# Kernel optimization log

Measured on AMD Instinct MI355X. Metric: run time of the kernel, lower is better.

## Reference

```python
import jax, jax.numpy as jnp
import numpy as np

N_NODES = 100000
D_IN = 128
D_OUT = 128
SHAPES = {"r1": 1, "r2": 2, "r3": 3}
N_EDGES = {"r1": 400000, "r2": 300000, "r3": 200000}


def setup_inputs() -> dict:
    key = jax.random.key(0)
    ks = jax.random.split(key, 10)
    inp = {
        "x": jax.random.normal(ks[0], (N_NODES, D_IN), dtype=jnp.float32),
        "A_r1": jax.random.normal(ks[1], (D_IN * 1, D_OUT), dtype=jnp.float32) * 0.05,
        "A_r2": jax.random.normal(ks[2], (D_IN * 2, D_OUT), dtype=jnp.float32) * 0.05,
        "A_r3": jax.random.normal(ks[3], (D_IN * 3, D_OUT), dtype=jnp.float32) * 0.05,
        "C_w": jax.random.normal(ks[4], (D_IN, D_OUT), dtype=jnp.float32) * 0.05,
        "C_b": jax.random.normal(ks[5], (D_OUT,), dtype=jnp.float32) * 0.05,
    }
    for j, (name, shape) in enumerate(SHAPES.items()):
        n = N_EDGES[name] * shape
        inp[f"ei_{name}"] = jax.random.randint(ks[6 + j], (2, n), 0, N_NODES, dtype=jnp.int64)
    return inp


def _edge_type_agg(x, edge_indices, A, shape):
    # edge_indices: [2, n_edges*shape]; row0 = sources, row1 reshaped -> dest per hyperedge
    dest = edge_indices[1].reshape(-1, shape)[:, 0]          # [n_edges]
    gathered = x[edge_indices[0]].reshape(-1, shape * x.shape[1])  # [n_edges, shape*D_IN]
    msg = gathered @ A                                        # [n_edges, D_OUT]
    # 1/count(dest) normalization (torch.unique counts == per-type in-degree)
    deg = jax.ops.segment_sum(jnp.ones_like(dest, dtype=msg.dtype), dest, num_segments=x.shape[0])
    msg = msg / deg[dest][:, None]
    return jax.ops.segment_sum(msg, dest, num_segments=x.shape[0])  # scatter_add


def reference(x, ei_r1, ei_r2, ei_r3, A_r1, A_r2, A_r3, C_w, C_b):
    agg = (_edge_type_agg(x, ei_r1, A_r1, 1)
           + _edge_type_agg(x, ei_r2, A_r2, 2)
           + _edge_type_agg(x, ei_r3, A_r3, 3))
    return x @ C_w + C_b + agg
```

## Files before the change

kernel.cpp:

```cpp
#include <hip/hip_runtime.h>

#define N_NODES 100000
#define D 128
#define NND 12800000
#define NTOT (3 * N_NODES)

typedef unsigned short u16;
typedef short s16x8 __attribute__((ext_vector_type(8)));
typedef float f32x4 __attribute__((ext_vector_type(4)));


__device__ __forceinline__ u16 f2b(float f) {
    union { float f; unsigned u; } v; v.f = f;
    unsigned r = (v.u + 0x7FFFu + ((v.u >> 16) & 1u)) >> 16;
    return (u16)r;
}


__global__ __launch_bounds__(256) void convert_all(
    const float* __restrict__ A1, const float* __restrict__ A2,
    const float* __restrict__ A3, const float* __restrict__ Cw,
    u16* __restrict__ ATb) {
    int m = blockIdx.x >> 6;
    int idx = (blockIdx.x & 63) * 256 + threadIdx.x;
    int n = idx >> 7, kk = idx & 127;
    const float* src; int srow;
    if (m == 0)      { src = Cw; srow = kk; }
    else if (m == 1) { src = A1; srow = kk; }
    else if (m < 4)  { src = A2; srow = (m - 2) * 128 + kk; }
    else             { src = A3; srow = (m - 4) * 128 + kk; }
    ATb[m * 16384 + n * 128 + kk] = f2b(src[(long)srow * 128 + n]);
}


__global__ __launch_bounds__(256) void zero_deg(int* deg, int n) {
    int i = blockIdx.x * 256 + threadIdx.x;
    if (i < n) deg[i] = 0;
}

__global__ __launch_bounds__(256) void deg_count(const int* __restrict__ ei, int n_edges,
                                                 int shape, int* __restrict__ deg) {
    int e = blockIdx.x * 256 + threadIdx.x;
    if (e < n_edges) {
        int dest = ei[(long)n_edges * shape + (long)e * shape];
        atomicAdd(&deg[dest], 1);
    }
}

__global__ __launch_bounds__(256) void scan_reduce(const int* __restrict__ deg,
                                                   int* __restrict__ bsums, int n) {
    __shared__ int s[256];
    int t = threadIdx.x;
    int base = blockIdx.x * 1024 + t * 4;
    int loc = 0;
#pragma unroll
    for (int r = 0; r < 4; r++) {
        int idx = base + r;
        if (idx < n) loc += deg[idx];
    }
    s[t] = loc;
    for (int off = 128; off > 0; off >>= 1) {
        __syncthreads();
        if (t < off) s[t] += s[t + off];
    }
    if (t == 0) bsums[blockIdx.x] = s[0];
}

__global__ __launch_bounds__(512) void scan_tops(const int* __restrict__ bsums,
                                                 int* __restrict__ boffs,
                                                 int* __restrict__ offs, int nb, int n) {
    __shared__ int s[512];
    int t = threadIdx.x;
    int v = (t < nb) ? bsums[t] : 0;
    s[t] = v;
    for (int off = 1; off < 512; off <<= 1) {
        __syncthreads();
        int x = (t >= off) ? s[t - off] : 0;
        __syncthreads();
        s[t] += x;
    }
    if (t < nb) boffs[t] = s[t] - v;
    if (t == nb - 1) offs[n] = s[t];
}

__global__ __launch_bounds__(256) void scan_final(const int* __restrict__ deg,
                                                  const int* __restrict__ boffs,
                                                  int* __restrict__ offs,
                                                  int* __restrict__ cursor, int n) {
    __shared__ int s[256];
    int t = threadIdx.x;
    int base = blockIdx.x * 1024 + t * 4;
    int v[4], p[4];
#pragma unroll
    for (int r = 0; r < 4; r++) {
        int idx = base + r;
        v[r] = (idx < n) ? deg[idx] : 0;
    }
    p[0] = 0; p[1] = v[0]; p[2] = v[0] + v[1]; p[3] = v[0] + v[1] + v[2];
    int tsum = p[3] + v[3];
    s[t] = tsum;
    for (int off = 1; off < 256; off <<= 1) {
        __syncthreads();
        int x = (t >= off) ? s[t - off] : 0;
        __syncthreads();
        s[t] += x;
    }
    int texcl = s[t] - tsum + boffs[blockIdx.x];
#pragma unroll
    for (int r = 0; r < 4; r++) {
        int idx = base + r;
        if (idx < n) {
            int val = texcl + p[r];
            offs[idx] = val;
            cursor[idx] = val;
        }
    }
}

template <int SHAPE>
__global__ __launch_bounds__(256) void scatter_src(const int* __restrict__ ei, int n_edges,
                                                   int* __restrict__ cursor, int base,
                                                   int* __restrict__ csr) {
    int e = blockIdx.x * 256 + threadIdx.x;
    if (e < n_edges) {
        int dest = ei[(long)n_edges * SHAPE + (long)e * SHAPE];
        int pos = atomicAdd(&cursor[dest], 1) - base;
#pragma unroll
        for (int s = 0; s < SHAPE; s++) csr[pos * SHAPE + s] = ei[(long)e * SHAPE + s];
    }
}


template <int NW, bool DENSE>
__global__ __launch_bounds__(256) void gemm_y(
    const float* __restrict__ x, const u16* __restrict__ AT,
    const float* __restrict__ Cb, u16* __restrict__ Yout, float* __restrict__ outf) {
    __shared__ u16 Xs[4][64][40];
    const int t = threadIdx.x;
    const int d0 = blockIdx.x * 64;

#pragma unroll
    for (int i = 0; i < 8; i++) {
        int f = i * 256 + t;
        int row = f >> 5;
        int k4 = f & 31;
        int rs = d0 + row < N_NODES ? d0 + row : N_NODES - 1;
        float4 v = *(const float4*)&x[(long)rs * D + k4 * 4];
        int chunk = k4 >> 3, kk = (k4 & 7) * 4;
        u16* p = &Xs[chunk][row][kk];
        p[0] = f2b(v.x); p[1] = f2b(v.y); p[2] = f2b(v.z); p[3] = f2b(v.w);
    }
    __syncthreads();

    const int lane = t & 63, wv = t >> 6;
    const int nbase = wv * 32, quad = lane >> 4, lrow = lane & 15;

    s16x8 afrag[4][4];
#pragma unroll
    for (int mi = 0; mi < 4; mi++)
#pragma unroll
        for (int c = 0; c < 4; c++)
            afrag[mi][c] = *(const s16x8*)&Xs[c][mi * 16 + lrow][quad * 8];

#pragma unroll
    for (int w = 0; w < NW; w++) {
        const u16* B = AT + w * 16384;
        s16x8 bfrag[2][4];
#pragma unroll
        for (int ni = 0; ni < 2; ni++)
#pragma unroll
            for (int c = 0; c < 4; c++)
                bfrag[ni][c] = *(const s16x8*)(B + (long)(nbase + ni * 16 + lrow) * 128 +
                                               c * 32 + quad * 8);
        f32x4 acc[4][2];
#pragma unroll
        for (int mi = 0; mi < 4; mi++)
#pragma unroll
            for (int ni = 0; ni < 2; ni++) acc[mi][ni] = (f32x4)(0.0f);
#pragma unroll
        for (int c = 0; c < 4; c++)
#pragma unroll
            for (int mi = 0; mi < 4; mi++)
#pragma unroll
                for (int ni = 0; ni < 2; ni++)
                    acc[mi][ni] = __builtin_amdgcn_mfma_f32_16x16x32_bf16(
                        afrag[mi][c], bfrag[ni][c], acc[mi][ni], 0, 0, 0);
#pragma unroll
        for (int mi = 0; mi < 4; mi++)
#pragma unroll
            for (int ni = 0; ni < 2; ni++)
#pragma unroll
                for (int reg = 0; reg < 4; reg++) {
                    int row = mi * 16 + quad * 4 + reg;
                    int col = nbase + ni * 16 + lrow;
                    if (d0 + row < N_NODES) {
                        long idx = (long)(d0 + row) * D + col;
                        if (DENSE) outf[idx] = acc[mi][ni][reg] + Cb[col];
                        else Yout[(long)w * NND + idx] = f2b(acc[mi][ni][reg]);
                    }
                }
    }
}


template <int SHAPE>
__global__ __launch_bounds__(256) void gather_acc(
    const u16* __restrict__ Y, const int* __restrict__ csr,
    const int* __restrict__ offs_t, int base, float* __restrict__ out) {
    const int lane = threadIdx.x & 63;
    int wid = blockIdx.x * 4 + (threadIdx.x >> 6);
    const int nw = gridDim.x * 4;
    for (int d = wid; d < N_NODES; d += nw) {
        int lo = offs_t[d] - base;
        int hi = offs_t[d + 1] - base;
        int cnt = hi - lo;
        if (cnt <= 0) continue;
        float a0 = 0.0f, a1 = 0.0f;
        int p = lo;
        for (; p + 4 <= hi; p += 4) {
            int sv[4][SHAPE];
#pragma unroll
            for (int i = 0; i < 4; i++)
#pragma unroll
                for (int s = 0; s < SHAPE; s++) sv[i][s] = csr[(p + i) * SHAPE + s];
            unsigned rw[4][SHAPE];
#pragma unroll
            for (int i = 0; i < 4; i++)
#pragma unroll
                for (int s = 0; s < SHAPE; s++)
                    rw[i][s] = *(const unsigned*)(Y + (long)s * NND +
                                                  (long)sv[i][s] * D + lane * 2);
#pragma unroll
            for (int i = 0; i < 4; i++)
#pragma unroll
                for (int s = 0; s < SHAPE; s++) {
                    a0 += __uint_as_float(rw[i][s] << 16);
                    a1 += __uint_as_float(rw[i][s] & 0xFFFF0000u);
                }
        }
        for (; p < hi; p++) {
            int sv[SHAPE];
#pragma unroll
            for (int s = 0; s < SHAPE; s++) sv[s] = csr[p * SHAPE + s];
#pragma unroll
            for (int s = 0; s < SHAPE; s++) {
                unsigned w = *(const unsigned*)(Y + (long)s * NND + (long)sv[s] * D + lane * 2);
                a0 += __uint_as_float(w << 16);
                a1 += __uint_as_float(w & 0xFFFF0000u);
            }
        }
        float inv = 1.0f / (float)cnt;
        float2* op = (float2*)&out[(long)d * D + lane * 2];
        float2 o = *op;
        o.x += a0 * inv;
        o.y += a1 * inv;
        *op = o;
    }
}


extern "C" void kernel_launch(void* const* d_in, const int* in_sizes, int n_in,
                              void* d_out, int out_size, void* d_ws, size_t ws_size,
                              hipStream_t stream) {
    const float* x  = (const float*)d_in[0];
    const float* A1 = (const float*)d_in[1];
    const float* A2 = (const float*)d_in[2];
    const float* A3 = (const float*)d_in[3];
    const float* Cw = (const float*)d_in[4];
    const float* Cb = (const float*)d_in[5];
    const int* e1 = (const int*)d_in[6];
    const int* e2 = (const int*)d_in[7];
    const int* e3 = (const int*)d_in[8];
    float* out = (float*)d_out;

    int* ws = (int*)d_ws;
    int* deg    = ws;
    int* offs   = ws + 300000;
    int* cursor = ws + 600001;
    int* csr1   = ws + 900001;
    int* csr2   = ws + 1300001;
    int* csr3   = ws + 1900001;
    int* bsums  = ws + 2500001;
    int* boffs  = ws + 2500513;

    u16* ATb = (u16*)((char*)d_ws + 10004224);
    u16* ATCw = ATb;
    u16* AT1  = ATb + 16384;
    u16* AT2  = ATb + 32768;
    u16* AT3  = ATb + 65536;
    u16* Y    = (u16*)((char*)d_ws + 10233600);

    const int NE1 = in_sizes[6] / 2;
    const int NE2 = in_sizes[7] / (2 * 2);
    const int NE3 = in_sizes[8] / (2 * 3);
    const int n = NTOT;
    const int NB = (n + 1023) / 1024;
    const int GB = (N_NODES + 63) / 64;

    convert_all<<<448, 256, 0, stream>>>(A1, A2, A3, Cw, ATb);

    zero_deg<<<(n + 255) / 256, 256, 0, stream>>>(deg, n);
    deg_count<<<(NE1 + 255) / 256, 256, 0, stream>>>(e1, NE1, 1, deg);
    deg_count<<<(NE2 + 255) / 256, 256, 0, stream>>>(e2, NE2, 2, deg + N_NODES);
    deg_count<<<(NE3 + 255) / 256, 256, 0, stream>>>(e3, NE3, 3, deg + 2 * N_NODES);

    scan_reduce<<<NB, 256, 0, stream>>>(deg, bsums, n);
    scan_tops<<<1, 512, 0, stream>>>(bsums, boffs, offs, NB, n);
    scan_final<<<NB, 256, 0, stream>>>(deg, boffs, offs, cursor, n);

    scatter_src<1><<<(NE1 + 255) / 256, 256, 0, stream>>>(e1, NE1, cursor, 0, csr1);
    scatter_src<2><<<(NE2 + 255) / 256, 256, 0, stream>>>(e2, NE2, cursor + N_NODES, NE1, csr2);
    scatter_src<3><<<(NE3 + 255) / 256, 256, 0, stream>>>(e3, NE3, cursor + 2 * N_NODES,
                                                          NE1 + NE2, csr3);

    gemm_y<1, true><<<GB, 256, 0, stream>>>(x, ATCw, Cb, nullptr, out);

    gemm_y<1, false><<<GB, 256, 0, stream>>>(x, AT1, nullptr, Y, nullptr);
    gather_acc<1><<<2048, 256, 0, stream>>>(Y, csr1, offs, 0, out);

    gemm_y<2, false><<<GB, 256, 0, stream>>>(x, AT2, nullptr, Y, nullptr);
    gather_acc<2><<<2048, 256, 0, stream>>>(Y, csr2, offs + N_NODES, NE1, out);

    gemm_y<3, false><<<GB, 256, 0, stream>>>(x, AT3, nullptr, Y, nullptr);
    gather_acc<3><<<2048, 256, 0, stream>>>(Y, csr3, offs + 2 * N_NODES, NE1 + NE2, out);
}
```

Baseline: 438.0 us.

## Unify per-type CSR into one weighted entry list and fuse GEMMs and gathers

Replaces the three per-type CSR builds, four GEMMs and three gather passes with one combined CSR per destination node. Each entry carries a precomputed 1/deg scale, and the x@C_w term is added as a self-entry with weight 1. A single GEMM kernel computes all seven weight slices and writes bf16 Y with coalesced stores staged through shared memory. A single gather then produces each output row in one write with the bias added. This removes repeated read-modify-write of the output, several kernel launches, and the fp32 dense GEMM output path. In exchange the dense C_w term is now rounded through bf16, entries are 8 bytes, and Y grows to seven slabs.

Result: faster. 356.6 us (-18.6%).

```diff
diff --git a/kernel.cpp b/kernel.cpp
--- a/kernel.cpp
+++ b/kernel.cpp
@@ -2,53 +2,73 @@
 
 #define N_NODES 100000
 #define D 128
-#define NND 12800000
-#define NTOT (3 * N_NODES)
+#define NND 12800000L
 
 typedef unsigned short u16;
 typedef short s16x8 __attribute__((ext_vector_type(8)));
 typedef float f32x4 __attribute__((ext_vector_type(4)));
 
+
+#define ENTS_OFF 2004160L
+#define AT_OFF   15604224L
+#define Y_OFF    15833600L
 
 __device__ __forceinline__ u16 f2b(float f) {
     union { float f; unsigned u; } v; v.f = f;
     unsigned r = (v.u + 0x7FFFu + ((v.u >> 16) & 1u)) >> 16;
     return (u16)r;
 }
-
-
-__global__ __launch_bounds__(256) void convert_all(
+__device__ __forceinline__ float blo(unsigned w) { return __uint_as_float(w << 16); }
+__device__ __forceinline__ float bhi(unsigned w) { return __uint_as_float(w & 0xFFFF0000u); }
+
+
+__global__ __launch_bounds__(256) void init_kernel(
     const float* __restrict__ A1, const float* __restrict__ A2,
     const float* __restrict__ A3, const float* __restrict__ Cw,
-    u16* __restrict__ ATb) {
-    int m = blockIdx.x >> 6;
-    int idx = (blockIdx.x & 63) * 256 + threadIdx.x;
+    u16* __restrict__ ATb, int* __restrict__ deg) {
+    int b = blockIdx.x, t = threadIdx.x;
+    if (b < 293) {
+        int i0 = (b * 256 + t) * 4;
+#pragma unroll
+        for (int r = 0; r < 4; r++)
+            if (i0 + r < 300000) deg[i0 + r] = 0;
+        return;
+    }
+    int mb = b - 293;
+    int m = mb >> 6;
+    int idx = (mb & 63) * 256 + t;
     int n = idx >> 7, kk = idx & 127;
     const float* src; int srow;
-    if (m == 0)      { src = Cw; srow = kk; }
-    else if (m == 1) { src = A1; srow = kk; }
-    else if (m < 4)  { src = A2; srow = (m - 2) * 128 + kk; }
-    else             { src = A3; srow = (m - 4) * 128 + kk; }
+    if (m == 0)      { src = A1; srow = kk; }
+    else if (m < 3)  { src = A2; srow = (m - 1) * 128 + kk; }
+    else if (m < 6)  { src = A3; srow = (m - 3) * 128 + kk; }
+    else             { src = Cw; srow = kk; }
     ATb[m * 16384 + n * 128 + kk] = f2b(src[(long)srow * 128 + n]);
 }
 
 
-__global__ __launch_bounds__(256) void zero_deg(int* deg, int n) {
-    int i = blockIdx.x * 256 + threadIdx.x;
-    if (i < n) deg[i] = 0;
-}
-
-__global__ __launch_bounds__(256) void deg_count(const int* __restrict__ ei, int n_edges,
-                                                 int shape, int* __restrict__ deg) {
-    int e = blockIdx.x * 256 + threadIdx.x;
-    if (e < n_edges) {
-        int dest = ei[(long)n_edges * shape + (long)e * shape];
-        atomicAdd(&deg[dest], 1);
-    }
-}
-
-__global__ __launch_bounds__(256) void scan_reduce(const int* __restrict__ deg,
-                                                   int* __restrict__ bsums, int n) {
+__global__ __launch_bounds__(256) void deg_all(
+    const int* __restrict__ e1, const int* __restrict__ e2, const int* __restrict__ e3,
+    int ne1, int ne2, int ne3, int* __restrict__ deg) {
+    int g = blockIdx.x * 256 + threadIdx.x;
+    if (g < ne1) {
+        atomicAdd(&deg[e1[ne1 + g]], 1);
+    } else if (g < ne1 + ne2) {
+        int e = g - ne1;
+        atomicAdd(&deg[N_NODES + e2[ne2 * 2 + e * 2]], 1);
+    } else if (g < ne1 + ne2 + ne3) {
+        int e = g - ne1 - ne2;
+        atomicAdd(&deg[2 * N_NODES + e3[ne3 * 3 + e * 3]], 1);
+    }
+}
+
+__device__ __forceinline__ int ucnt(const int* deg, int d) {
+    return 1 + deg[d] + 2 * deg[N_NODES + d] + 3 * deg[2 * N_NODES + d];
+}
+
+
+__global__ __launch_bounds__(256) void scan_reduce_u(const int* __restrict__ deg,
+                                                     int* __restrict__ bsums, int n) {
     __shared__ int s[256];
     int t = threadIdx.x;
     int base = blockIdx.x * 1024 + t * 4;
@@ -56,7 +76,7 @@
 #pragma unroll
     for (int r = 0; r < 4; r++) {
         int idx = base + r;
-        if (idx < n) loc += deg[idx];
+        if (idx < n) loc += ucnt(deg, idx);
     }
     s[t] = loc;
     for (int off = 128; off > 0; off >>= 1) {
@@ -83,10 +103,9 @@
     if (t == nb - 1) offs[n] = s[t];
 }
 
-__global__ __launch_bounds__(256) void scan_final(const int* __restrict__ deg,
-                                                  const int* __restrict__ boffs,
-                                                  int* __restrict__ offs,
-                                                  int* __restrict__ cursor, int n) {
+__global__ __launch_bounds__(256) void scan_final_u(
+    const int* __restrict__ deg, const int* __restrict__ boffs,
+    int* __restrict__ offs, int* __restrict__ cursor, int2* __restrict__ ents, int n) {
     __shared__ int s[256];
     int t = threadIdx.x;
     int base = blockIdx.x * 1024 + t * 4;
@@ -94,7 +113,7 @@
 #pragma unroll
     for (int r = 0; r < 4; r++) {
         int idx = base + r;
-        v[r] = (idx < n) ? deg[idx] : 0;
+        v[r] = (idx < n) ? ucnt(deg, idx) : 0;
     }
     p[0] = 0; p[1] = v[0]; p[2] = v[0] + v[1]; p[3] = v[0] + v[1] + v[2];
     int tsum = p[3] + v[3];
@@ -112,30 +131,48 @@
         if (idx < n) {
             int val = texcl + p[r];
             offs[idx] = val;
-            cursor[idx] = val;
+            cursor[idx] = val + 1;
+            ents[val] = make_int2(6 * N_NODES + idx, __float_as_int(1.0f));
         }
     }
 }
 
-template <int SHAPE>
-__global__ __launch_bounds__(256) void scatter_src(const int* __restrict__ ei, int n_edges,
-                                                   int* __restrict__ cursor, int base,
-                                                   int* __restrict__ csr) {
-    int e = blockIdx.x * 256 + threadIdx.x;
-    if (e < n_edges) {
-        int dest = ei[(long)n_edges * SHAPE + (long)e * SHAPE];
-        int pos = atomicAdd(&cursor[dest], 1) - base;
-#pragma unroll
-        for (int s = 0; s < SHAPE; s++) csr[pos * SHAPE + s] = ei[(long)e * SHAPE + s];
-    }
-}
-
-
-template <int NW, bool DENSE>
-__global__ __launch_bounds__(256) void gemm_y(
-    const float* __restrict__ x, const u16* __restrict__ AT,
-    const float* __restrict__ Cb, u16* __restrict__ Yout, float* __restrict__ outf) {
-    __shared__ u16 Xs[4][64][40];
+
+__global__ __launch_bounds__(256) void scatter_all(
+    const int* __restrict__ e1, const int* __restrict__ e2, const int* __restrict__ e3,
+    int ne1, int ne2, int ne3, const int* __restrict__ deg,
+    int* __restrict__ cursor, int2* __restrict__ ents) {
+    int g = blockIdx.x * 256 + threadIdx.x;
+    if (g < ne1) {
+        int dest = e1[ne1 + g];
+        float sc = 1.0f / (float)deg[dest];
+        int pos = atomicAdd(&cursor[dest], 1);
+        ents[pos] = make_int2(e1[g], __float_as_int(sc));
+    } else if (g < ne1 + ne2) {
+        int e = g - ne1;
+        int dest = e2[ne2 * 2 + e * 2];
+        float sc = 1.0f / (float)deg[N_NODES + dest];
+        int pos = atomicAdd(&cursor[dest], 2);
+        ents[pos]     = make_int2(1 * N_NODES + e2[e * 2],     __float_as_int(sc));
+        ents[pos + 1] = make_int2(2 * N_NODES + e2[e * 2 + 1], __float_as_int(sc));
+    } else if (g < ne1 + ne2 + ne3) {
+        int e = g - ne1 - ne2;
+        int dest = e3[ne3 * 3 + e * 3];
+        float sc = 1.0f / (float)deg[2 * N_NODES + dest];
+        int pos = atomicAdd(&cursor[dest], 3);
+#pragma unroll
+        for (int s = 0; s < 3; s++)
+            ents[pos + s] = make_int2((3 + s) * N_NODES + e3[e * 3 + s], __float_as_int(sc));
+    }
+}
+
+
+__global__ __launch_bounds__(256) void gemm_all(
+    const float* __restrict__ x, const u16* __restrict__ AT, u16* __restrict__ Y) {
+    __shared__ float smemf[64 * 132];
+    typedef u16 XsT[64][40];
+    XsT* Xs = reinterpret_cast<XsT*>(smemf);
+
     const int t = threadIdx.x;
     const int d0 = blockIdx.x * 64;
 
@@ -162,8 +199,7 @@
         for (int c = 0; c < 4; c++)
             afrag[mi][c] = *(const s16x8*)&Xs[c][mi * 16 + lrow][quad * 8];
 
-#pragma unroll
-    for (int w = 0; w < NW; w++) {
+    for (int w = 0; w < 7; w++) {
         const u16* B = AT + w * 16384;
         s16x8 bfrag[2][4];
 #pragma unroll
@@ -185,6 +221,8 @@
                 for (int ni = 0; ni < 2; ni++)
                     acc[mi][ni] = __builtin_amdgcn_mfma_f32_16x16x32_bf16(
                         afrag[mi][c], bfrag[ni][c], acc[mi][ni], 0, 0, 0);
+
+        __syncthreads();
 #pragma unroll
         for (int mi = 0; mi < 4; mi++)
 #pragma unroll
@@ -193,68 +231,62 @@
                 for (int reg = 0; reg < 4; reg++) {
                     int row = mi * 16 + quad * 4 + reg;
                     int col = nbase + ni * 16 + lrow;
-                    if (d0 + row < N_NODES) {
-                        long idx = (long)(d0 + row) * D + col;
-                        if (DENSE) outf[idx] = acc[mi][ni][reg] + Cb[col];
-                        else Yout[(long)w * NND + idx] = f2b(acc[mi][ni][reg]);
-                    }
+                    smemf[row * 132 + col] = acc[mi][ni][reg];
                 }
-    }
-}
-
-
-template <int SHAPE>
-__global__ __launch_bounds__(256) void gather_acc(
-    const u16* __restrict__ Y, const int* __restrict__ csr,
-    const int* __restrict__ offs_t, int base, float* __restrict__ out) {
-    const int lane = threadIdx.x & 63;
-    int wid = blockIdx.x * 4 + (threadIdx.x >> 6);
-    const int nw = gridDim.x * 4;
-    for (int d = wid; d < N_NODES; d += nw) {
-        int lo = offs_t[d] - base;
-        int hi = offs_t[d + 1] - base;
-        int cnt = hi - lo;
-        if (cnt <= 0) continue;
-        float a0 = 0.0f, a1 = 0.0f;
-        int p = lo;
-        for (; p + 4 <= hi; p += 4) {
-            int sv[4][SHAPE];
-#pragma unroll
-            for (int i = 0; i < 4; i++)
-#pragma unroll
-                for (int s = 0; s < SHAPE; s++) sv[i][s] = csr[(p + i) * SHAPE + s];
-            unsigned rw[4][SHAPE];
-#pragma unroll
-            for (int i = 0; i < 4; i++)
-#pragma unroll
-                for (int s = 0; s < SHAPE; s++)
-                    rw[i][s] = *(const unsigned*)(Y + (long)s * NND +
-                                                  (long)sv[i][s] * D + lane * 2);
-#pragma unroll
-            for (int i = 0; i < 4; i++)
-#pragma unroll
-                for (int s = 0; s < SHAPE; s++) {
-                    a0 += __uint_as_float(rw[i][s] << 16);
-                    a1 += __uint_as_float(rw[i][s] & 0xFFFF0000u);
-                }
-        }
-        for (; p < hi; p++) {
-            int sv[SHAPE];
-#pragma unroll
-            for (int s = 0; s < SHAPE; s++) sv[s] = csr[p * SHAPE + s];
-#pragma unroll
-            for (int s = 0; s < SHAPE; s++) {
-                unsigned w = *(const unsigned*)(Y + (long)s * NND + (long)sv[s] * D + lane * 2);
-                a0 += __uint_as_float(w << 16);
-                a1 += __uint_as_float(w & 0xFFFF0000u);
+        __syncthreads();
+        u16* Yw = Y + (long)w * NND;
+#pragma unroll
+        for (int i = 0; i < 8; i++) {
+            int f = i * 256 + t;
+            int row = f >> 5;
+            int col = (f & 31) * 4;
+            if (d0 + row < N_NODES) {
+                float4 v = *(const float4*)&smemf[row * 132 + col];
+                unsigned o0 = (unsigned)f2b(v.x) | ((unsigned)f2b(v.y) << 16);
+                unsigned o1 = (unsigned)f2b(v.z) | ((unsigned)f2b(v.w) << 16);
+                uint2 o = make_uint2(o0, o1);
+                *(uint2*)(Yw + (long)(d0 + row) * D + col) = o;
             }
         }
-        float inv = 1.0f / (float)cnt;
-        float2* op = (float2*)&out[(long)d * D + lane * 2];
-        float2 o = *op;
-        o.x += a0 * inv;
-        o.y += a1 * inv;
-        *op = o;
+        __syncthreads();
+    }
+}
+
+
+__global__ __launch_bounds__(256) void gather_all(
+    const u16* __restrict__ Y, const int2* __restrict__ ents,
+    const int* __restrict__ offs, const float* __restrict__ Cb,
+    float* __restrict__ out) {
+    const int lane = threadIdx.x & 63;
+    const int wv = __builtin_amdgcn_readfirstlane(threadIdx.x >> 6);
+    int wid = blockIdx.x * 4 + wv;
+    const int nw = gridDim.x * 4;
+    const float cb0 = Cb[lane * 2];
+    const float cb1 = Cb[lane * 2 + 1];
+
+    for (int d = wid; d < N_NODES; d += nw) {
+        int lo = offs[d];
+        int hi = offs[d + 1];
+        float a0 = 0.0f, a1 = 0.0f;
+        for (int p = lo; p < hi; p += 8) {
+            int2 e[8];
+#pragma unroll
+            for (int i = 0; i < 8; i++) {
+                int q = p + i;
+                e[i] = ents[q < hi ? q : hi - 1];
+            }
+            unsigned w[8];
+#pragma unroll
+            for (int i = 0; i < 8; i++)
+                w[i] = *(const unsigned*)(Y + (long)e[i].x * D + lane * 2);
+#pragma unroll
+            for (int i = 0; i < 8; i++) {
+                float s = (p + i < hi) ? __int_as_float(e[i].y) : 0.0f;
+                a0 = fmaf(s, blo(w[i]), a0);
+                a1 = fmaf(s, bhi(w[i]), a1);
+            }
+        }
+        *(float2*)&out[(long)d * D + lane * 2] = make_float2(a0 + cb0, a1 + cb1);
     }
 }
 
@@ -276,51 +308,27 @@
     int* ws = (int*)d_ws;
     int* deg    = ws;
     int* offs   = ws + 300000;
-    int* cursor = ws + 600001;
-    int* csr1   = ws + 900001;
-    int* csr2   = ws + 1300001;
-    int* csr3   = ws + 1900001;
-    int* bsums  = ws + 2500001;
-    int* boffs  = ws + 2500513;
-
-    u16* ATb = (u16*)((char*)d_ws + 10004224);
-    u16* ATCw = ATb;
-    u16* AT1  = ATb + 16384;
-    u16* AT2  = ATb + 32768;
-    u16* AT3  = ATb + 65536;
-    u16* Y    = (u16*)((char*)d_ws + 10233600);
+    int* cursor = ws + 400001;
+    int* bsums  = ws + 500001;
+    int* boffs  = ws + 500513;
+    int2* ents  = (int2*)((char*)d_ws + ENTS_OFF);
+    u16* ATb    = (u16*)((char*)d_ws + AT_OFF);
+    u16* Y      = (u16*)((char*)d_ws + Y_OFF);
 
     const int NE1 = in_sizes[6] / 2;
     const int NE2 = in_sizes[7] / (2 * 2);
     const int NE3 = in_sizes[8] / (2 * 3);
-    const int n = NTOT;
+    const int NET = NE1 + NE2 + NE3;
+    const int n = N_NODES;
     const int NB = (n + 1023) / 1024;
-    const int GB = (N_NODES + 63) / 64;
-
-    convert_all<<<448, 256, 0, stream>>>(A1, A2, A3, Cw, ATb);
-
-    zero_deg<<<(n + 255) / 256, 256, 0, stream>>>(deg, n);
-    deg_count<<<(NE1 + 255) / 256, 256, 0, stream>>>(e1, NE1, 1, deg);
-    deg_count<<<(NE2 + 255) / 256, 256, 0, stream>>>(e2, NE2, 2, deg + N_NODES);
-    deg_count<<<(NE3 + 255) / 256, 256, 0, stream>>>(e3, NE3, 3, deg + 2 * N_NODES);
-
-    scan_reduce<<<NB, 256, 0, stream>>>(deg, bsums, n);
+
+    init_kernel<<<293 + 448, 256, 0, stream>>>(A1, A2, A3, Cw, ATb, deg);
+    deg_all<<<(NET + 255) / 256, 256, 0, stream>>>(e1, e2, e3, NE1, NE2, NE3, deg);
+    scan_reduce_u<<<NB, 256, 0, stream>>>(deg, bsums, n);
     scan_tops<<<1, 512, 0, stream>>>(bsums, boffs, offs, NB, n);
-    scan_final<<<NB, 256, 0, stream>>>(deg, boffs, offs, cursor, n);
-
-    scatter_src<1><<<(NE1 + 255) / 256, 256, 0, stream>>>(e1, NE1, cursor, 0, csr1);
-    scatter_src<2><<<(NE2 + 255) / 256, 256, 0, stream>>>(e2, NE2, cursor + N_NODES, NE1, csr2);
-    scatter_src<3><<<(NE3 + 255) / 256, 256, 0, stream>>>(e3, NE3, cursor + 2 * N_NODES,
-                                                          NE1 + NE2, csr3);
-
-    gemm_y<1, true><<<GB, 256, 0, stream>>>(x, ATCw, Cb, nullptr, out);
-
-    gemm_y<1, false><<<GB, 256, 0, stream>>>(x, AT1, nullptr, Y, nullptr);
-    gather_acc<1><<<2048, 256, 0, stream>>>(Y, csr1, offs, 0, out);
-
-    gemm_y<2, false><<<GB, 256, 0, stream>>>(x, AT2, nullptr, Y, nullptr);
-    gather_acc<2><<<2048, 256, 0, stream>>>(Y, csr2, offs + N_NODES, NE1, out);
-
-    gemm_y<3, false><<<GB, 256, 0, stream>>>(x, AT3, nullptr, Y, nullptr);
-    gather_acc<3><<<2048, 256, 0, stream>>>(Y, csr3, offs + 2 * N_NODES, NE1 + NE2, out);
-}
+    scan_final_u<<<NB, 256, 0, stream>>>(deg, boffs, offs, cursor, ents, n);
+    scatter_all<<<(NET + 255) / 256, 256, 0, stream>>>(e1, e2, e3, NE1, NE2, NE3,
+                                                       deg, cursor, ents);
+    gemm_all<<<(N_NODES + 63) / 64, 256, 0, stream>>>(x, ATb, Y);
+    gather_all<<<2048, 256, 0, stream>>>(Y, ents, offs, Cb, out);
+}
```
